# Optimization experiments

Measured on AMD Instinct MI355X. Metric: run time of the kernel, lower is better.

Reference implementation:

```python
import jax, jax.numpy as jnp
import numpy as np

HIDDEN = 1024
HEADS = 16
D_HEAD = HIDDEN // HEADS  # 64
B, S = 4, 1024


def setup_inputs() -> dict:
    key = jax.random.key(0)
    ks = jax.random.split(key, 12)
    p = 0.02  # param init scale
    inp = {
        "q": jax.random.normal(ks[0], (B, S, HIDDEN), jnp.float32),
        "k": jax.random.normal(ks[1], (B, S, HIDDEN), jnp.float32),
        "v": jax.random.normal(ks[2], (B, S, HIDDEN), jnp.float32),
        "attn_bias": jax.random.normal(ks[3], (B, HEADS, S, S), jnp.float32),
        # Linear weights stored as [in, out] (equivalent to torch's x @ W.T)
        "Wq": jax.random.normal(ks[4], (HIDDEN, HIDDEN), jnp.float32) * p,
        "Wk": jax.random.normal(ks[5], (HIDDEN, HIDDEN), jnp.float32) * p,
        "Wv": jax.random.normal(ks[6], (HIDDEN, HIDDEN), jnp.float32) * p,
        "Wo": jax.random.normal(ks[7], (HIDDEN, HIDDEN), jnp.float32) * p,
        "bq": jax.random.normal(ks[8], (HIDDEN,), jnp.float32) * p,
        "bk": jax.random.normal(ks[9], (HIDDEN,), jnp.float32) * p,
        "bv": jax.random.normal(ks[10], (HIDDEN,), jnp.float32) * p,
        "bo": jax.random.normal(ks[11], (HIDDEN,), jnp.float32) * p,
    }
    return inp


def reference(q, k, v, attn_bias, Wq, Wk, Wv, Wo, bq, bk, bv, bo):
    b, s, _ = q.shape
    scale = D_HEAD ** (-0.5)
    # projections -> [b, heads, s, d]
    qh = (q @ Wq + bq).reshape(b, s, HEADS, D_HEAD).transpose(0, 2, 1, 3)
    kh = (k @ Wk + bk).reshape(b, s, HEADS, D_HEAD).transpose(0, 2, 1, 3)
    vh = (v @ Wv + bv).reshape(b, s, HEADS, D_HEAD).transpose(0, 2, 1, 3)
    # scaled scores + additive bias, softmax over keys
    scores = jnp.einsum("bhqd,bhkd->bhqk", qh * scale, kh) + attn_bias
    attn = jax.nn.softmax(scores, axis=-1)  # dropout rate is 0.0
    ctx = jnp.einsum("bhqk,bhkd->bhqd", attn, vh)
    ctx = ctx.transpose(0, 2, 1, 3).reshape(b, s, HIDDEN)
    return ctx @ Wo + bo
```

## Files before the change

### kernel.cpp

```cpp
#include <hip/hip_runtime.h>
#include <stdint.h>

#define HID 1024
#define NH 16
#define DH 64
#define NB 4
#define SQL 1024
#define MROWS (NB*SQL)

typedef unsigned short u16;
typedef __attribute__((ext_vector_type(8))) short short8;
typedef __attribute__((ext_vector_type(4))) float f32x4;

__device__ __forceinline__ u16 f2bf(float f){
  union { float f; uint32_t u; } v; v.f = f;
  uint32_t u = v.u;
  u += 0x7FFF + ((u >> 16) & 1);
  return (u16)(u >> 16);
}

__device__ __forceinline__ void gld_lds16(const u16* g, u16* l){
  __builtin_amdgcn_global_load_lds((const __attribute__((address_space(1))) void*)g,
                                   (__attribute__((address_space(3))) void*)l, 16, 0, 0);
}

__global__ __launch_bounds__(256) void cvt_bf16(const float* __restrict__ in,
                                                u16* __restrict__ out, int n){
  int idx = (blockIdx.x*256 + threadIdx.x)*4;
  if (idx < n){
    float4 f = *(const float4*)(in + idx);
    u16 o0=f2bf(f.x), o1=f2bf(f.y), o2=f2bf(f.z), o3=f2bf(f.w);
    ushort4 o; o.x=o0; o.y=o1; o.z=o2; o.w=o3;
    *(ushort4*)(out+idx) = o;
  }
}

__global__ __launch_bounds__(256) void transpose_w(const float* __restrict__ W,
                                                   u16* __restrict__ Wt){
  __shared__ __align__(16) u16 tile[64][65];
  const int t = threadIdx.x;
  const int r0 = blockIdx.y*64, c0 = blockIdx.x*64;
  #pragma unroll
  for (int i=0;i<16;i++){
    int idx = i*256 + t; int r = idx>>6, c = idx&63;
    tile[r][c] = f2bf(W[(size_t)(r0+r)*HID + c0 + c]);
  }
  __syncthreads();
  #pragma unroll
  for (int i=0;i<16;i++){
    int idx = i*256 + t; int n = idx>>6, k = idx&63;
    Wt[(size_t)(c0+n)*HID + r0 + k] = tile[k][n];
  }
}

template<int MODE>
__global__ __launch_bounds__(256) void gemm_bt(const u16* __restrict__ A,
    const u16* __restrict__ Bt, const float* __restrict__ bias,
    void* __restrict__ outp){
  __shared__ __align__(16) u16 As[128*64];
  __shared__ __align__(16) u16 Bs[128*64];
  const int t = threadIdx.x;
  const int n0 = blockIdx.x*128, m0 = blockIdx.y*128;
  const int w = t>>6, lane = t&63, lr = lane&15, lhi = lane>>4;
  const int wr = w>>1, wc = w&1;
  const int K = HID;

  f32x4 acc[4][4];
  #pragma unroll
  for (int i=0;i<4;i++)
    #pragma unroll
    for (int j=0;j<4;j++) acc[i][j] = 0.0f;

  for (int kt=0; kt<K/64; ++kt){
    __syncthreads();
    const u16* Ag = A + (size_t)m0*K + kt*64;
    const u16* Bg = Bt + (size_t)n0*K + kt*64;
    #pragma unroll
    for (int i=0;i<4;i++){
      int seg = i*256 + t;
      gld_lds16(Ag + (seg>>3)*K + (seg&7)*8, As + seg*8);
    }
    #pragma unroll
    for (int i=0;i<4;i++){
      int seg = i*256 + t;
      gld_lds16(Bg + (seg>>3)*K + (seg&7)*8, Bs + seg*8);
    }
    __syncthreads();
    #pragma unroll
    for (int sl=0; sl<2; ++sl){
      short8 af[4], bf[4];
      #pragma unroll
      for (int mi=0;mi<4;mi++)
        af[mi] = *(const short8*)(As + (wr*64 + mi*16 + lr)*64 + sl*32 + lhi*8);
      #pragma unroll
      for (int ni=0;ni<4;ni++)
        bf[ni] = *(const short8*)(Bs + (wc*64 + ni*16 + lr)*64 + sl*32 + lhi*8);
      #pragma unroll
      for (int mi=0;mi<4;mi++)
        #pragma unroll
        for (int ni=0;ni<4;ni++)
          acc[mi][ni] = __builtin_amdgcn_mfma_f32_16x16x32_bf16(af[mi], bf[ni], acc[mi][ni], 0,0,0);
    }
  }

  #pragma unroll
  for (int mi=0;mi<4;mi++){
    #pragma unroll
    for (int ni=0;ni<4;ni++){
      const int n = n0 + wc*64 + ni*16 + lr;
      const int mbase = m0 + wr*64 + mi*16 + lhi*4;
      const float bv = bias[n];
      #pragma unroll
      for (int r=0;r<4;r++){
        const int m = mbase + r;
        float val = acc[mi][ni][r] + bv;
        if (MODE == 2){
          ((float*)outp)[(size_t)m*HID + n] = val;
        } else {
          int b = m >> 10, s = m & 1023;
          int h = n >> 6,  d = n & 63;
          if (MODE == 0)
            ((u16*)outp)[(((size_t)(b*NH + h))*SQL + s)*DH + d] = f2bf(val);
          else
            ((u16*)outp)[(((size_t)(b*NH + h))*DH + d)*SQL + s] = f2bf(val);
        }
      }
    }
  }
}

__global__ __launch_bounds__(256) void attn_fwd(const u16* __restrict__ Qh,
    const u16* __restrict__ Kh, const u16* __restrict__ Vt,
    const float* __restrict__ bias, u16* __restrict__ ctx){
  __shared__ __align__(16) u16 Ks[64*64];
  __shared__ __align__(16) u16 Vs[64*64];
  __shared__ __align__(16) u16 Ps[4*16*64];
  const int t = threadIdx.x, w = t>>6, lane = t&63, lr = lane&15, lhi = lane>>4;
  const int q0 = blockIdx.x*64;
  const int bh = blockIdx.y;
  const int b = bh >> 4, h = bh & 15;
  const u16* Qp = Qh + (size_t)bh*SQL*DH;
  const u16* Kp = Kh + (size_t)bh*SQL*DH;
  const u16* Vp = Vt + (size_t)bh*DH*SQL;
  const float* Bp = bias + ((size_t)bh*SQL + q0)*SQL;

  short8 qf[2];
  {
    const int qrow = q0 + w*16 + lr;
    qf[0] = *(const short8*)(Qp + qrow*DH + lhi*8);
    qf[1] = *(const short8*)(Qp + qrow*DH + 32 + lhi*8);
  }

  float m_run[4], l_run[4];
  f32x4 o[4];
  #pragma unroll
  for (int r=0;r<4;r++){ m_run[r] = -3.0e38f; l_run[r] = 0.0f; }
  #pragma unroll
  for (int dg=0;dg<4;dg++) o[dg] = 0.0f;

  for (int kt=0; kt<SQL/64; ++kt){
    __syncthreads();
    #pragma unroll
    for (int i=0;i<2;i++){
      int seg = i*256 + t;
      gld_lds16(Kp + (kt*64 + (seg>>3))*DH + (seg&7)*8, Ks + seg*8);
    }
    #pragma unroll
    for (int i=0;i<2;i++){
      int seg = i*256 + t;
      gld_lds16(Vp + (size_t)(seg>>3)*SQL + kt*64 + (seg&7)*8, Vs + seg*8);
    }
    __syncthreads();

    f32x4 sa[4];
    #pragma unroll
    for (int n=0;n<4;n++) sa[n] = 0.0f;
    #pragma unroll
    for (int sl=0; sl<2; ++sl){
      #pragma unroll
      for (int n=0;n<4;n++){
        short8 kf = *(const short8*)(Ks + (n*16+lr)*64 + sl*32 + lhi*8);
        sa[n] = __builtin_amdgcn_mfma_f32_16x16x32_bf16(qf[sl], kf, sa[n], 0,0,0);
      }
    }
    float sv[4][4];
    #pragma unroll
    for (int n=0;n<4;n++)
      #pragma unroll
      for (int r=0;r<4;r++){
        float bvv = Bp[(size_t)(w*16 + lhi*4 + r)*SQL + kt*64 + n*16 + lr];
        sv[n][r] = sa[n][r]*0.125f + bvv;
      }

    float tmax[4];
    #pragma unroll
    for (int r=0;r<4;r++)
      tmax[r] = fmaxf(fmaxf(sv[0][r],sv[1][r]), fmaxf(sv[2][r],sv[3][r]));
    #pragma unroll
    for (int off=1; off<16; off<<=1)
      #pragma unroll
      for (int r=0;r<4;r++)
        tmax[r] = fmaxf(tmax[r], __shfl_xor(tmax[r], off, 64));

    float alpha[4], rsum[4];
    #pragma unroll
    for (int r=0;r<4;r++){
      float mnew = fmaxf(m_run[r], tmax[r]);
      alpha[r] = __expf(m_run[r] - mnew);
      m_run[r] = mnew;
      rsum[r] = 0.0f;
    }
    #pragma unroll
    for (int n=0;n<4;n++)
      #pragma unroll
      for (int r=0;r<4;r++){
        float p = __expf(sv[n][r] - m_run[r]);
        sv[n][r] = p;
        rsum[r] += p;
      }
    #pragma unroll
    for (int off=1; off<16; off<<=1)
      #pragma unroll
      for (int r=0;r<4;r++)
        rsum[r] += __shfl_xor(rsum[r], off, 64);
    #pragma unroll
    for (int r=0;r<4;r++) l_run[r] = l_run[r]*alpha[r] + rsum[r];
    #pragma unroll
    for (int dg=0;dg<4;dg++)
      #pragma unroll
      for (int r=0;r<4;r++) o[dg][r] *= alpha[r];

    u16* Pw = Ps + w*(16*64);
    #pragma unroll
    for (int n=0;n<4;n++)
      #pragma unroll
      for (int r=0;r<4;r++)
        Pw[(lhi*4 + r)*64 + n*16 + lr] = f2bf(sv[n][r]);
    asm volatile("s_waitcnt lgkmcnt(0)" ::: "memory");

    #pragma unroll
    for (int sl=0; sl<2; ++sl){
      short8 pf = *(const short8*)(Pw + lr*64 + sl*32 + lhi*8);
      #pragma unroll
      for (int dg=0; dg<4; dg++){
        short8 vf = *(const short8*)(Vs + (dg*16+lr)*64 + sl*32 + lhi*8);
        o[dg] = __builtin_amdgcn_mfma_f32_16x16x32_bf16(pf, vf, o[dg], 0,0,0);
      }
    }
  }

  #pragma unroll
  for (int dg=0; dg<4; dg++)
    #pragma unroll
    for (int r=0;r<4;r++){
      float val = o[dg][r] / l_run[r];
      int srow = q0 + w*16 + lhi*4 + r;
      ctx[((size_t)b*SQL + srow)*HID + h*64 + dg*16 + lr] = f2bf(val);
    }
}

extern "C" void kernel_launch(void* const* d_in, const int* in_sizes, int n_in,
                              void* d_out, int out_size, void* d_ws, size_t ws_size,
                              hipStream_t stream){
  const float* q  = (const float*)d_in[0];
  const float* k  = (const float*)d_in[1];
  const float* v  = (const float*)d_in[2];
  const float* ab = (const float*)d_in[3];
  const float* Wq = (const float*)d_in[4];
  const float* Wk = (const float*)d_in[5];
  const float* Wv = (const float*)d_in[6];
  const float* Wo = (const float*)d_in[7];
  const float* bq = (const float*)d_in[8];
  const float* bk = (const float*)d_in[9];
  const float* bv = (const float*)d_in[10];
  const float* bo = (const float*)d_in[11];

  char* ws = (char*)d_ws;
  const size_t MB = 1024*1024;
  u16* qb  = (u16*)(ws + 0*MB);
  u16* kb  = (u16*)(ws + 8*MB);
  u16* vb  = (u16*)(ws + 16*MB);
  u16* wqt = (u16*)(ws + 24*MB);
  u16* wkt = (u16*)(ws + 26*MB);
  u16* wvt = (u16*)(ws + 28*MB);
  u16* wot = (u16*)(ws + 30*MB);
  u16* Qh  = (u16*)(ws + 32*MB);
  u16* Kh  = (u16*)(ws + 40*MB);
  u16* Vt  = (u16*)(ws + 48*MB);
  u16* ctx = (u16*)(ws + 56*MB);

  const int NEL = MROWS*HID;
  dim3 cb(256), cg(NEL/4/256);
  cvt_bf16<<<cg, cb, 0, stream>>>(q, qb, NEL);
  cvt_bf16<<<cg, cb, 0, stream>>>(k, kb, NEL);
  cvt_bf16<<<cg, cb, 0, stream>>>(v, vb, NEL);

  dim3 tg(16,16);
  transpose_w<<<tg, cb, 0, stream>>>(Wq, wqt);
  transpose_w<<<tg, cb, 0, stream>>>(Wk, wkt);
  transpose_w<<<tg, cb, 0, stream>>>(Wv, wvt);
  transpose_w<<<tg, cb, 0, stream>>>(Wo, wot);

  dim3 gg(HID/128, MROWS/128);
  gemm_bt<0><<<gg, cb, 0, stream>>>(qb, wqt, bq, (void*)Qh);
  gemm_bt<0><<<gg, cb, 0, stream>>>(kb, wkt, bk, (void*)Kh);
  gemm_bt<1><<<gg, cb, 0, stream>>>(vb, wvt, bv, (void*)Vt);

  dim3 ag(SQL/64, NB*NH);
  attn_fwd<<<ag, cb, 0, stream>>>(Qh, Kh, Vt, ab, ctx);

  gemm_bt<2><<<gg, cb, 0, stream>>>(ctx, wot, bo, d_out);
}
```

Before: 583.5 us.

## Batch launches, double-buffer GEMM and attention tiles, swizzle attention LDS

Merges the three input conversions, four weight transposes and three QKV projections into single batched launches using a grid dimension. Double-buffers the GEMM LDS tiles so the next K tile's global-to-LDS load overlaps the current MFMA work. In attention, K/V tiles are prefetched into registers and written to a second LDS buffer after compute, the bias loads are issued early, and the K, V and P layouts in LDS get an XOR swizzle to avoid bank conflicts. The cost is more LDS per block, which may lower occupancy, and the GEMM mode becomes a runtime value instead of a template parameter.

```diff
diff --git a/kernel.cpp b/kernel.cpp
--- a/kernel.cpp
+++ b/kernel.cpp
@@ -24,19 +24,24 @@
                                    (__attribute__((address_space(3))) void*)l, 16, 0, 0);
 }
 
-__global__ __launch_bounds__(256) void cvt_bf16(const float* __restrict__ in,
-                                                u16* __restrict__ out, int n){
+__global__ __launch_bounds__(256) void cvt_bf16_3(const float* __restrict__ s0,
+    const float* __restrict__ s1, const float* __restrict__ s2,
+    u16* __restrict__ d0, u16* __restrict__ d1, u16* __restrict__ d2){
+  const float* src = (blockIdx.y==0) ? s0 : (blockIdx.y==1) ? s1 : s2;
+  u16* dst = (blockIdx.y==0) ? d0 : (blockIdx.y==1) ? d1 : d2;
   int idx = (blockIdx.x*256 + threadIdx.x)*4;
-  if (idx < n){
-    float4 f = *(const float4*)(in + idx);
-    u16 o0=f2bf(f.x), o1=f2bf(f.y), o2=f2bf(f.z), o3=f2bf(f.w);
-    ushort4 o; o.x=o0; o.y=o1; o.z=o2; o.w=o3;
-    *(ushort4*)(out+idx) = o;
-  }
-}
-
-__global__ __launch_bounds__(256) void transpose_w(const float* __restrict__ W,
-                                                   u16* __restrict__ Wt){
+  float4 f = *(const float4*)(src + idx);
+  ushort4 o; o.x=f2bf(f.x); o.y=f2bf(f.y); o.z=f2bf(f.z); o.w=f2bf(f.w);
+  *(ushort4*)(dst+idx) = o;
+}
+
+__global__ __launch_bounds__(256) void transpose_w4(
+    const float* __restrict__ W0, const float* __restrict__ W1,
+    const float* __restrict__ W2, const float* __restrict__ W3,
+    u16* __restrict__ T0, u16* __restrict__ T1,
+    u16* __restrict__ T2, u16* __restrict__ T3){
+  const float* W = (blockIdx.z==0)?W0:(blockIdx.z==1)?W1:(blockIdx.z==2)?W2:W3;
+  u16* Wt = (blockIdx.z==0)?T0:(blockIdx.z==1)?T1:(blockIdx.z==2)?T2:T3;
   __shared__ __align__(16) u16 tile[64][65];
   const int t = threadIdx.x;
   const int r0 = blockIdx.y*64, c0 = blockIdx.x*64;
@@ -53,17 +58,15 @@
   }
 }
 
-template<int MODE>
-__global__ __launch_bounds__(256) void gemm_bt(const u16* __restrict__ A,
+__device__ __forceinline__ void gemm_core(const u16* __restrict__ A,
     const u16* __restrict__ Bt, const float* __restrict__ bias,
-    void* __restrict__ outp){
-  __shared__ __align__(16) u16 As[128*64];
-  __shared__ __align__(16) u16 Bs[128*64];
+    void* __restrict__ outp, int mode){
+  __shared__ __align__(16) u16 As[2][128*64];
+  __shared__ __align__(16) u16 Bs[2][128*64];
   const int t = threadIdx.x;
   const int n0 = blockIdx.x*128, m0 = blockIdx.y*128;
   const int w = t>>6, lane = t&63, lr = lane&15, lhi = lane>>4;
   const int wr = w>>1, wc = w&1;
-  const int K = HID;
 
   f32x4 acc[4][4];
   #pragma unroll
@@ -71,36 +74,54 @@
     #pragma unroll
     for (int j=0;j<4;j++) acc[i][j] = 0.0f;
 
-  for (int kt=0; kt<K/64; ++kt){
-    __syncthreads();
-    const u16* Ag = A + (size_t)m0*K + kt*64;
-    const u16* Bg = Bt + (size_t)n0*K + kt*64;
-    #pragma unroll
-    for (int i=0;i<4;i++){
-      int seg = i*256 + t;
-      gld_lds16(Ag + (seg>>3)*K + (seg&7)*8, As + seg*8);
-    }
-    #pragma unroll
-    for (int i=0;i<4;i++){
-      int seg = i*256 + t;
-      gld_lds16(Bg + (seg>>3)*K + (seg&7)*8, Bs + seg*8);
-    }
-    __syncthreads();
+  const u16* Ag0 = A + (size_t)m0*HID;
+  const u16* Bg0 = Bt + (size_t)n0*HID;
+
+  #pragma unroll
+  for (int i=0;i<4;i++){
+    int seg = i*256 + t;
+    gld_lds16(Ag0 + (size_t)(seg>>3)*HID + (seg&7)*8, &As[0][seg*8]);
+  }
+  #pragma unroll
+  for (int i=0;i<4;i++){
+    int seg = i*256 + t;
+    gld_lds16(Bg0 + (size_t)(seg>>3)*HID + (seg&7)*8, &Bs[0][seg*8]);
+  }
+  __syncthreads();
+
+  int cur = 0;
+  for (int kt=0; kt<HID/64; ++kt){
+    if (kt+1 < HID/64){
+      const u16* Ag = Ag0 + (kt+1)*64;
+      const u16* Bg = Bg0 + (kt+1)*64;
+      #pragma unroll
+      for (int i=0;i<4;i++){
+        int seg = i*256 + t;
+        gld_lds16(Ag + (size_t)(seg>>3)*HID + (seg&7)*8, &As[cur^1][seg*8]);
+      }
+      #pragma unroll
+      for (int i=0;i<4;i++){
+        int seg = i*256 + t;
+        gld_lds16(Bg + (size_t)(seg>>3)*HID + (seg&7)*8, &Bs[cur^1][seg*8]);
+      }
+    }
     #pragma unroll
     for (int sl=0; sl<2; ++sl){
       short8 af[4], bf[4];
       #pragma unroll
       for (int mi=0;mi<4;mi++)
-        af[mi] = *(const short8*)(As + (wr*64 + mi*16 + lr)*64 + sl*32 + lhi*8);
+        af[mi] = *(const short8*)(&As[cur][(wr*64 + mi*16 + lr)*64 + sl*32 + lhi*8]);
       #pragma unroll
       for (int ni=0;ni<4;ni++)
-        bf[ni] = *(const short8*)(Bs + (wc*64 + ni*16 + lr)*64 + sl*32 + lhi*8);
+        bf[ni] = *(const short8*)(&Bs[cur][(wc*64 + ni*16 + lr)*64 + sl*32 + lhi*8]);
       #pragma unroll
       for (int mi=0;mi<4;mi++)
         #pragma unroll
         for (int ni=0;ni<4;ni++)
           acc[mi][ni] = __builtin_amdgcn_mfma_f32_16x16x32_bf16(af[mi], bf[ni], acc[mi][ni], 0,0,0);
     }
+    __syncthreads();
+    cur ^= 1;
   }
 
   #pragma unroll
@@ -114,12 +135,12 @@
       for (int r=0;r<4;r++){
         const int m = mbase + r;
         float val = acc[mi][ni][r] + bv;
-        if (MODE == 2){
+        if (mode == 2){
           ((float*)outp)[(size_t)m*HID + n] = val;
         } else {
           int b = m >> 10, s = m & 1023;
           int h = n >> 6,  d = n & 63;
-          if (MODE == 0)
+          if (mode == 0)
             ((u16*)outp)[(((size_t)(b*NH + h))*SQL + s)*DH + d] = f2bf(val);
           else
             ((u16*)outp)[(((size_t)(b*NH + h))*DH + d)*SQL + s] = f2bf(val);
@@ -129,11 +150,29 @@
   }
 }
 
+__global__ __launch_bounds__(256) void gemm_qkv(
+    const u16* __restrict__ qA, const u16* __restrict__ kA, const u16* __restrict__ vA,
+    const u16* __restrict__ Wq, const u16* __restrict__ Wk, const u16* __restrict__ Wv,
+    const float* __restrict__ bq, const float* __restrict__ bk, const float* __restrict__ bv,
+    u16* __restrict__ Qh, u16* __restrict__ Kh, u16* __restrict__ Vt){
+  int z = blockIdx.z;
+  const u16* A  = (z==0)?qA:(z==1)?kA:vA;
+  const u16* Bt = (z==0)?Wq:(z==1)?Wk:Wv;
+  const float* bias = (z==0)?bq:(z==1)?bk:bv;
+  u16* out = (z==0)?Qh:(z==1)?Kh:Vt;
+  gemm_core(A, Bt, bias, (void*)out, (z==2)?1:0);
+}
+
+__global__ __launch_bounds__(256) void gemm_o(const u16* __restrict__ A,
+    const u16* __restrict__ Bt, const float* __restrict__ bias, float* __restrict__ out){
+  gemm_core(A, Bt, bias, (void*)out, 2);
+}
+
 __global__ __launch_bounds__(256) void attn_fwd(const u16* __restrict__ Qh,
     const u16* __restrict__ Kh, const u16* __restrict__ Vt,
     const float* __restrict__ bias, u16* __restrict__ ctx){
-  __shared__ __align__(16) u16 Ks[64*64];
-  __shared__ __align__(16) u16 Vs[64*64];
+  __shared__ __align__(16) u16 Ks[2][64*64];
+  __shared__ __align__(16) u16 Vs[2][64*64];
   __shared__ __align__(16) u16 Ps[4*16*64];
   const int t = threadIdx.x, w = t>>6, lane = t&63, lr = lane&15, lhi = lane>>4;
   const int q0 = blockIdx.x*64;
@@ -144,11 +183,16 @@
   const u16* Vp = Vt + (size_t)bh*DH*SQL;
   const float* Bp = bias + ((size_t)bh*SQL + q0)*SQL;
 
+  const int srow0 = t>>3,        scol0 = t&7;
+  const int srow1 = 32 + (t>>3), scol1 = t&7;
+  const int ldso0 = srow0*64 + ((scol0*8) ^ ((srow0&7)<<3));
+  const int ldso1 = srow1*64 + ((scol1*8) ^ ((srow1&7)<<3));
+
   short8 qf[2];
   {
     const int qrow = q0 + w*16 + lr;
-    qf[0] = *(const short8*)(Qp + qrow*DH + lhi*8);
-    qf[1] = *(const short8*)(Qp + qrow*DH + 32 + lhi*8);
+    qf[0] = *(const short8*)(Qp + (size_t)qrow*DH + lhi*8);
+    qf[1] = *(const short8*)(Qp + (size_t)qrow*DH + 32 + lhi*8);
   }
 
   float m_run[4], l_run[4];
@@ -158,28 +202,46 @@
   #pragma unroll
   for (int dg=0;dg<4;dg++) o[dg] = 0.0f;
 
+  {
+    short8 k0 = *(const short8*)(Kp + (size_t)srow0*DH + scol0*8);
+    short8 k1 = *(const short8*)(Kp + (size_t)srow1*DH + scol1*8);
+    short8 v0 = *(const short8*)(Vp + (size_t)srow0*SQL + scol0*8);
+    short8 v1 = *(const short8*)(Vp + (size_t)srow1*SQL + scol1*8);
+    *(short8*)(&Ks[0][ldso0]) = k0;
+    *(short8*)(&Ks[0][ldso1]) = k1;
+    *(short8*)(&Vs[0][ldso0]) = v0;
+    *(short8*)(&Vs[0][ldso1]) = v1;
+  }
+  __syncthreads();
+
+  int cur = 0;
   for (int kt=0; kt<SQL/64; ++kt){
-    __syncthreads();
-    #pragma unroll
-    for (int i=0;i<2;i++){
-      int seg = i*256 + t;
-      gld_lds16(Kp + (kt*64 + (seg>>3))*DH + (seg&7)*8, Ks + seg*8);
-    }
-    #pragma unroll
-    for (int i=0;i<2;i++){
-      int seg = i*256 + t;
-      gld_lds16(Vp + (size_t)(seg>>3)*SQL + kt*64 + (seg&7)*8, Vs + seg*8);
-    }
-    __syncthreads();
+    short8 kreg0, kreg1, vreg0, vreg1;
+    const bool pre = (kt+1 < SQL/64);
+    if (pre){
+      const int kn = (kt+1)*64;
+      kreg0 = *(const short8*)(Kp + (size_t)(kn + srow0)*DH + scol0*8);
+      kreg1 = *(const short8*)(Kp + (size_t)(kn + srow1)*DH + scol1*8);
+      vreg0 = *(const short8*)(Vp + (size_t)srow0*SQL + kn + scol0*8);
+      vreg1 = *(const short8*)(Vp + (size_t)srow1*SQL + kn + scol1*8);
+    }
+
+    float bvv[4][4];
+    #pragma unroll
+    for (int n=0;n<4;n++)
+      #pragma unroll
+      for (int r=0;r<4;r++)
+        bvv[n][r] = Bp[(size_t)(w*16 + lhi*4 + r)*SQL + kt*64 + n*16 + lr];
 
     f32x4 sa[4];
     #pragma unroll
     for (int n=0;n<4;n++) sa[n] = 0.0f;
     #pragma unroll
     for (int sl=0; sl<2; ++sl){
+      const int co = (sl*32 + lhi*8) ^ ((lr&7)<<3);
       #pragma unroll
       for (int n=0;n<4;n++){
-        short8 kf = *(const short8*)(Ks + (n*16+lr)*64 + sl*32 + lhi*8);
+        short8 kf = *(const short8*)(&Ks[cur][(n*16+lr)*64 + co]);
         sa[n] = __builtin_amdgcn_mfma_f32_16x16x32_bf16(qf[sl], kf, sa[n], 0,0,0);
       }
     }
@@ -187,10 +249,8 @@
     #pragma unroll
     for (int n=0;n<4;n++)
       #pragma unroll
-      for (int r=0;r<4;r++){
-        float bvv = Bp[(size_t)(w*16 + lhi*4 + r)*SQL + kt*64 + n*16 + lr];
-        sv[n][r] = sa[n][r]*0.125f + bvv;
-      }
+      for (int r=0;r<4;r++)
+        sv[n][r] = sa[n][r]*0.125f + bvv[n][r];
 
     float tmax[4];
     #pragma unroll
@@ -234,19 +294,33 @@
     #pragma unroll
     for (int n=0;n<4;n++)
       #pragma unroll
-      for (int r=0;r<4;r++)
-        Pw[(lhi*4 + r)*64 + n*16 + lr] = f2bf(sv[n][r]);
+      for (int r=0;r<4;r++){
+        const int prow = lhi*4 + r;
+        Pw[prow*64 + ((n*16+lr) ^ ((prow&7)<<3))] = f2bf(sv[n][r]);
+      }
     asm volatile("s_waitcnt lgkmcnt(0)" ::: "memory");
+    __builtin_amdgcn_sched_barrier(0);
 
     #pragma unroll
     for (int sl=0; sl<2; ++sl){
-      short8 pf = *(const short8*)(Pw + lr*64 + sl*32 + lhi*8);
+      const int co = (sl*32 + lhi*8) ^ ((lr&7)<<3);
+      short8 pf = *(const short8*)(Pw + lr*64 + co);
       #pragma unroll
       for (int dg=0; dg<4; dg++){
-        short8 vf = *(const short8*)(Vs + (dg*16+lr)*64 + sl*32 + lhi*8);
+        short8 vf = *(const short8*)(&Vs[cur][(dg*16+lr)*64 + co]);
         o[dg] = __builtin_amdgcn_mfma_f32_16x16x32_bf16(pf, vf, o[dg], 0,0,0);
       }
     }
+
+    if (pre){
+      const int nb = cur^1;
+      *(short8*)(&Ks[nb][ldso0]) = kreg0;
+      *(short8*)(&Ks[nb][ldso1]) = kreg1;
+      *(short8*)(&Vs[nb][ldso0]) = vreg0;
+      *(short8*)(&Vs[nb][ldso1]) = vreg1;
+    }
+    __syncthreads();
+    cur ^= 1;
   }
 
   #pragma unroll
@@ -289,25 +363,19 @@
   u16* Vt  = (u16*)(ws + 48*MB);
   u16* ctx = (u16*)(ws + 56*MB);
 
-  const int NEL = MROWS*HID;
-  dim3 cb(256), cg(NEL/4/256);
-  cvt_bf16<<<cg, cb, 0, stream>>>(q, qb, NEL);
-  cvt_bf16<<<cg, cb, 0, stream>>>(k, kb, NEL);
-  cvt_bf16<<<cg, cb, 0, stream>>>(v, vb, NEL);
-
-  dim3 tg(16,16);
-  transpose_w<<<tg, cb, 0, stream>>>(Wq, wqt);
-  transpose_w<<<tg, cb, 0, stream>>>(Wk, wkt);
-  transpose_w<<<tg, cb, 0, stream>>>(Wv, wvt);
-  transpose_w<<<tg, cb, 0, stream>>>(Wo, wot);
-
-  dim3 gg(HID/128, MROWS/128);
-  gemm_bt<0><<<gg, cb, 0, stream>>>(qb, wqt, bq, (void*)Qh);
-  gemm_bt<0><<<gg, cb, 0, stream>>>(kb, wkt, bk, (void*)Kh);
-  gemm_bt<1><<<gg, cb, 0, stream>>>(vb, wvt, bv, (void*)Vt);
+  dim3 cb(256);
+  dim3 cg(MROWS*HID/4/256, 3);
+  cvt_bf16_3<<<cg, cb, 0, stream>>>(q, k, v, qb, kb, vb);
+
+  dim3 tg(16,16,4);
+  transpose_w4<<<tg, cb, 0, stream>>>(Wq, Wk, Wv, Wo, wqt, wkt, wvt, wot);
+
+  dim3 gq(HID/128, MROWS/128, 3);
+  gemm_qkv<<<gq, cb, 0, stream>>>(qb, kb, vb, wqt, wkt, wvt, bq, bk, bv, Qh, Kh, Vt);
 
   dim3 ag(SQL/64, NB*NH);
   attn_fwd<<<ag, cb, 0, stream>>>(Qh, Kh, Vt, ab, ctx);
 
-  gemm_bt<2><<<gg, cb, 0, stream>>>(ctx, wot, bo, d_out);
-}
+  dim3 gg(HID/128, MROWS/128);
+  gemm_o<<<gg, cb, 0, stream>>>(ctx, wot, bo, (float*)d_out);
+}
```

Measured after the change: 558.8 us. 1.04x faster.
